# Optimization experiments

Hardware: AMD Instinct MI355X
Metric: run time of the kernel (lower is better)

The kernel has to match this reference:

```python
import jax, jax.numpy as jnp
import numpy as np

SR = 48000
TIME_LENGTH = 62400  # int(1.3 * 48000)
MAX_VOICES = 16


def _conv1d_same(x, k, b):
    # x: [B, L, Cin], k: [K, Cin, Cout] -> [B, L, Cout], keras Conv1D padding='same'
    y = jax.lax.conv_general_dilated(x, k, (1,), 'SAME', dimension_numbers=('NWC', 'WIO', 'NWC'))
    return y + b


def setup_inputs() -> dict:
    key = jax.random.key(0)
    ks = jax.random.split(key, 20)
    B, L, D, C = 16, 250, 128, 32
    V = MAX_VOICES
    din = D + C
    w = lambda k, s: jax.random.normal(k, s, jnp.float32) * 0.05
    inp = {}
    inp['base_signal'] = jax.random.normal(ks[0], (B, TIME_LENGTH), jnp.float32)
    inp['z'] = jax.random.normal(ks[1], (B, L, D), jnp.float32)
    inp['cond'] = jax.random.uniform(ks[2], (B, C), jnp.float32)
    inp['fundamental_freq'] = jax.random.uniform(ks[3], (B,), jnp.float32)
    # param_predictor: Dense(256)->Dense(128)->Dense(64)->Dense(4)
    inp['W1'] = w(ks[4], (din, 256)); inp['b1'] = jnp.zeros((256,), jnp.float32)
    inp['W2'] = w(ks[5], (256, 128)); inp['b2'] = jnp.zeros((128,), jnp.float32)
    inp['W3'] = w(ks[6], (128, 64));  inp['b3'] = jnp.zeros((64,), jnp.float32)
    inp['W4'] = w(ks[7], (64, 4));    inp['b4'] = jnp.zeros((4,), jnp.float32)
    # voice_gain_net: Conv1D(128,7)->Conv1D(64,5)->Conv1D(V,3), input channels = D + C
    inp['K1'] = w(ks[8], (7, din, 128)); inp['cb1'] = jnp.zeros((128,), jnp.float32)
    inp['K2'] = w(ks[9], (5, 128, 64));  inp['cb2'] = jnp.zeros((64,), jnp.float32)
    inp['K3'] = w(ks[10], (3, 64, V));   inp['cb3'] = jnp.zeros((V,), jnp.float32)
    return inp


def reference(base_signal, z, cond, fundamental_freq,
              W1, b1, W2, b2, W3, b3, W4, b4,
              K1, cb1, K2, cb2, K3, cb3):
    B, T = base_signal.shape
    L = z.shape[1]
    V = MAX_VOICES
    # ---- global param predictor ----
    z_global = jnp.mean(z, axis=1)
    x = jnp.concatenate([z_global, cond], axis=-1)
    h = jax.nn.relu(x @ W1 + b1)
    h = jax.nn.relu(h @ W2 + b2)
    h = jax.nn.relu(h @ W3 + b3)
    params = h @ W4 + b4  # [B,4]
    num_voices = 1.0 + 14.0 * jax.nn.sigmoid(params[:, 0:1])  # [B,1]
    detune_cents = params[:, 1:2] * 50.0                       # [B,1] (unused downstream, as in source)
    spread = jax.nn.sigmoid(params[:, 2:3])                    # [B,1]
    depth = jax.nn.sigmoid(params[:, 3:4]) * 0.5               # [B,1]
    # ---- per-voice gain envelopes at latent rate ----
    z_cond = jnp.concatenate([z, jnp.broadcast_to(cond[:, None, :], (B, L, cond.shape[-1]))], axis=-1)
    g = jax.nn.relu(_conv1d_same(z_cond, K1, cb1))
    g = jax.nn.relu(_conv1d_same(g, K2, cb2))
    g = _conv1d_same(g, K3, cb3)  # [B, L, V]
    # TF bilinear resize (half-pixel centers) L -> T along time axis
    scale = L / T
    src = jnp.clip((jnp.arange(T, dtype=jnp.float32) + 0.5) * scale - 0.5, 0.0, L - 1.0)
    i0 = jnp.floor(src).astype(jnp.int32)
    i1 = jnp.minimum(i0 + 1, L - 1)
    frac = (src - i0.astype(jnp.float32))[None, :, None]
    vg = g[:, i0, :] * (1.0 - frac) + g[:, i1, :] * frac
    voice_gains = jax.nn.softplus(vg)  # [B, T, V]
    # ---- 16-voice detune/roll/LFO-modulate/accumulate, vectorized over voices ----
    pos = (np.arange(V) - (V - 1) / 2.0) / V            # static [V]
    shifts = np.trunc(pos * 20.0).astype(np.int64)      # int() truncation as in source
    gidx = (np.arange(T)[None, :] - shifts[:, None]) % T  # static [V, T] gather for tf.roll
    shifted = base_signal[:, jnp.asarray(gidx)]         # [B, V, T]
    t = jnp.arange(T, dtype=jnp.float32) / SR
    lfo_freq = 3.0 + 0.3 * jnp.arange(V, dtype=jnp.float32)
    lfo = jnp.sin(2.0 * np.pi * lfo_freq[:, None] * t[None, :])  # [V, T]
    modulated = shifted * (1.0 + 0.2 * depth[:, 0][:, None, None] * lfo[None])  # [B, V, T]
    pan = 1.0 - jnp.abs(jnp.asarray(pos, dtype=jnp.float32))[None, :] * spread * 0.5  # [B, V]
    unison = jnp.einsum('bvt,btv,bv->bt', modulated, voice_gains, pan)  # [B, T]
    # ---- soft voice-count mask and normalization ----
    voice_mask = jax.nn.sigmoid((num_voices - jnp.arange(V, dtype=jnp.float32)[None, :]) * 2.0)  # [B, V]
    norm = jnp.sqrt(jnp.sum(voice_mask, axis=-1, keepdims=True) + 1e-6)  # [B, 1]
    gain_sum = jnp.einsum('btv,bv->bt', voice_gains, voice_mask)  # [B, T]
    return gain_sum / (norm + 1e-6) * unison
```

## Files before the change

### kernel.cpp

```cpp
#include <hip/hip_runtime.h>
#include <hip/hip_bf16.h>
#include <math.h>

#define L_LEN 250
#define D_DIM 128
#define C_DIM 32
#define DIN   160
#define NV    16
#define T_LEN 62400

__global__ __launch_bounds__(256) void zmean_kernel(const float* __restrict__ z,
                                                    float* __restrict__ zpart) {
    int b = blockIdx.x / 10, s = blockIdx.x % 10;
    int l0 = s * 25;
    int tid = threadIdx.x;
    int d4 = tid & 31, rg = tid >> 5;
    float4 acc = make_float4(0.f, 0.f, 0.f, 0.f);
    const float4* zp = (const float4*)(z + ((size_t)b * L_LEN + l0) * D_DIM) + d4;
    for (int r = rg; r < 25; r += 8) {
        float4 v = zp[(size_t)r * 32];
        acc.x += v.x; acc.y += v.y; acc.z += v.z; acc.w += v.w;
    }
    __shared__ float4 sm[8][32];
    sm[rg][d4] = acc;
    __syncthreads();
    if (rg == 0) {
        #pragma unroll
        for (int g = 1; g < 8; ++g) {
            float4 v = sm[g][d4];
            acc.x += v.x; acc.y += v.y; acc.z += v.z; acc.w += v.w;
        }
        ((float4*)(zpart + ((size_t)b * 10 + s) * 128))[d4] = acc;
    }
}

__global__ __launch_bounds__(256) void conv1_mlp_kernel(
        const float* __restrict__ z, const float* __restrict__ cond,
        const float* __restrict__ K1, float* __restrict__ parts1,
        const float* __restrict__ zpart,
        const float* __restrict__ W1, const float* __restrict__ b1,
        const float* __restrict__ W2, const float* __restrict__ b2,
        const float* __restrict__ W3, const float* __restrict__ b3,
        const float* __restrict__ W4, const float* __restrict__ b4,
        float* __restrict__ P) {
    int tid = threadIdx.x;
    if (blockIdx.x >= 1024) {
        int b = blockIdx.x - 1024;
        __shared__ float xb[DIN];
        __shared__ float h1[256];
        __shared__ float h2[128];
        __shared__ float h3[64];
        __shared__ float pr[4];
        if (tid < 128) {
            float s = 0.f;
            const float* zp = zpart + (size_t)b * 10 * 128 + tid;
            #pragma unroll
            for (int q = 0; q < 10; ++q) s += zp[q * 128];
            xb[tid] = s * (1.0f / (float)L_LEN);
        } else if (tid < DIN) {
            xb[tid] = cond[b * C_DIM + (tid - 128)];
        }
        __syncthreads();
        {
            float a0 = b1[tid], a1 = 0.f;
            #pragma unroll 8
            for (int i = 0; i < DIN; i += 2) {
                a0 = fmaf(xb[i],     W1[i * 256 + tid],       a0);
                a1 = fmaf(xb[i + 1], W1[(i + 1) * 256 + tid], a1);
            }
            h1[tid] = fmaxf(a0 + a1, 0.f);
        }
        __syncthreads();
        if (tid < 128) {
            float a0 = b2[tid], a1 = 0.f;
            #pragma unroll 8
            for (int i = 0; i < 256; i += 2) {
                a0 = fmaf(h1[i],     W2[i * 128 + tid],       a0);
                a1 = fmaf(h1[i + 1], W2[(i + 1) * 128 + tid], a1);
            }
            h2[tid] = fmaxf(a0 + a1, 0.f);
        }
        __syncthreads();
        if (tid < 64) {
            float a0 = b3[tid], a1 = 0.f;
            #pragma unroll 8
            for (int i = 0; i < 128; i += 2) {
                a0 = fmaf(h2[i],     W3[i * 64 + tid],       a0);
                a1 = fmaf(h2[i + 1], W3[(i + 1) * 64 + tid], a1);
            }
            h3[tid] = fmaxf(a0 + a1, 0.f);
        }
        __syncthreads();
        if (tid < 4) {
            float acc = b4[tid];
            #pragma unroll 8
            for (int i = 0; i < 64; ++i) acc = fmaf(h3[i], W4[i * 4 + tid], acc);
            pr[tid] = acc;
        }
        __syncthreads();
        if (tid == 0) {
            float num_voices = 1.0f + 14.0f / (1.0f + __expf(-pr[0]));
            float spread     = 1.0f / (1.0f + __expf(-pr[2]));
            float depth      = 0.5f / (1.0f + __expf(-pr[3]));
            float* Pb = P + b * 40;
            float msum = 0.f;
            for (int v = 0; v < NV; ++v) {
                float m = 1.0f / (1.0f + __expf(-(num_voices - (float)v) * 2.0f));
                msum += m;
                Pb[2 + v] = m;
                float pos = ((float)v - 7.5f) * (1.0f / 16.0f);
                Pb[2 + NV + v] = 1.0f - fabsf(pos) * spread * 0.5f;
            }
            float norm = sqrtf(msum + 1e-6f);
            Pb[0] = depth;
            Pb[1] = 1.0f / (norm + 1e-6f);
        }
        return;
    }
    int blk = blockIdx.x;
    int s  = blk >> 8;
    int b  = (blk >> 4) & 15;
    int lt = blk & 15;
    int l0 = lt * 16;
    __shared__ float smc[40][28];
    for (int idx = tid; idx < 22 * 40; idx += 256) {
        int pl = idx / 40;
        int il = idx - pl * 40;
        int p  = l0 - 3 + pl;
        int gi = s * 40 + il;
        float v = 0.f;
        if (p >= 0 && p < L_LEN)
            v = (gi < D_DIM) ? z[((size_t)b * L_LEN + p) * D_DIM + gi]
                             : cond[b * C_DIM + (gi - D_DIM)];
        smc[il][pl] = v;
    }
    __syncthreads();
    int oc = tid & 127;
    int lb = (tid >> 7) * 8;
    float acc[8];
    #pragma unroll
    for (int j = 0; j < 8; ++j) acc[j] = 0.f;
    const float* kbase = K1 + (size_t)(s * 40) * 128 + oc;
    for (int il = 0; il < 40; ++il) {
        float zr[16];
        *(float4*)&zr[0]  = *(const float4*)&smc[il][lb];
        *(float4*)&zr[4]  = *(const float4*)&smc[il][lb + 4];
        *(float4*)&zr[8]  = *(const float4*)&smc[il][lb + 8];
        *(float4*)&zr[12] = *(const float4*)&smc[il][lb + 12];
        const float* kp = kbase + (size_t)il * 128;
        #pragma unroll
        for (int tap = 0; tap < 7; ++tap) {
            float k = kp[(size_t)tap * DIN * 128];
            #pragma unroll
            for (int j = 0; j < 8; ++j) acc[j] = fmaf(zr[tap + j], k, acc[j]);
        }
    }
    float* po = parts1 + (size_t)s * (16 * L_LEN * 128) + ((size_t)b * L_LEN) * 128 + oc;
    #pragma unroll
    for (int j = 0; j < 8; ++j) {
        int l = l0 + lb + j;
        if (l < L_LEN) po[(size_t)l * 128] = acc[j];
    }
}

__global__ __launch_bounds__(256) void conv2_split_kernel(
        const float* __restrict__ parts1, const float* __restrict__ cb1,
        const float* __restrict__ K2, float* __restrict__ parts2) {
    int blk = blockIdx.x;
    int h  = blk >> 8;
    int b  = (blk >> 4) & 15;
    int lt = blk & 15;
    int l0 = lt * 16;
    int tid = threadIdx.x;
    const int PSTR = 16 * L_LEN * 128;
    __shared__ float sm[64][28];
    for (int idx = tid; idx < 20 * 64; idx += 256) {
        int pl = idx >> 6;
        int il = idx & 63;
        int p  = l0 - 2 + pl;
        int gi = h * 64 + il;
        float v = 0.f;
        if (p >= 0 && p < L_LEN) {
            size_t o = ((size_t)b * L_LEN + p) * 128 + gi;
            v = cb1[gi] + parts1[o] + parts1[o + PSTR] + parts1[o + 2 * PSTR] + parts1[o + 3 * PSTR];
            v = fmaxf(v, 0.f);
        }
        sm[il][pl] = v;
    }
    __syncthreads();
    int oc = tid & 63;
    int lb = (tid >> 6) * 4;
    float acc[4];
    #pragma unroll
    for (int j = 0; j < 4; ++j) acc[j] = 0.f;
    const float* kbase = K2 + (size_t)(h * 64) * 64 + oc;
    for (int il = 0; il < 64; ++il) {
        float zr[8];
        *(float4*)&zr[0] = *(const float4*)&sm[il][lb];
        *(float4*)&zr[4] = *(const float4*)&sm[il][lb + 4];
        const float* kp = kbase + (size_t)il * 64;
        #pragma unroll
        for (int tap = 0; tap < 5; ++tap) {
            float k = kp[(size_t)tap * 128 * 64];
            #pragma unroll
            for (int j = 0; j < 4; ++j) acc[j] = fmaf(zr[tap + j], k, acc[j]);
        }
    }
    float* po = parts2 + (size_t)h * (16 * L_LEN * 64) + ((size_t)b * L_LEN) * 64 + oc;
    #pragma unroll
    for (int j = 0; j < 4; ++j) {
        int l = l0 + lb + j;
        if (l < L_LEN) po[(size_t)l * 64] = acc[j];
    }
}

__global__ __launch_bounds__(256) void conv3_kernel(
        const float* __restrict__ parts2, const float* __restrict__ cb2,
        const float* __restrict__ K3, const float* __restrict__ cb3,
        float* __restrict__ g3) {
    int b  = blockIdx.x >> 4;
    int lt = blockIdx.x & 15;
    int l0 = lt * 16;
    int tid = threadIdx.x;
    const int PSTR2 = 16 * L_LEN * 64;
    __shared__ float sm2[18][68];
    __shared__ float k3t[16][196];
    for (int idx = tid; idx < 3 * 64 * 16; idx += 256) {
        int v  = idx & 15;
        int ti = idx >> 4;
        k3t[v][ti] = K3[ti * 16 + v];
    }
    for (int idx = tid; idx < 18 * 64; idx += 256) {
        int pl = idx >> 6;
        int i  = idx & 63;
        int p  = l0 - 1 + pl;
        float v = 0.f;
        if (p >= 0 && p < L_LEN) {
            size_t o = ((size_t)b * L_LEN + p) * 64 + i;
            v = fmaxf(cb2[i] + parts2[o] + parts2[o + PSTR2], 0.f);
        }
        sm2[pl][i] = v;
    }
    __syncthreads();
    int v  = tid & 15;
    int lq = tid >> 4;
    int l  = l0 + lq;
    float acc = cb3[v];
    #pragma unroll
    for (int tap = 0; tap < 3; ++tap) {
        #pragma unroll
        for (int i4 = 0; i4 < 16; ++i4) {
            float4 g = *(const float4*)&sm2[lq + tap][i4 * 4];
            float4 k = *(const float4*)&k3t[v][tap * 64 + i4 * 4];
            acc = fmaf(g.x, k.x, acc);
            acc = fmaf(g.y, k.y, acc);
            acc = fmaf(g.z, k.z, acc);
            acc = fmaf(g.w, k.w, acc);
        }
    }
    if (l < L_LEN) g3[((size_t)b * L_LEN + l) * NV + v] = acc;
}

__global__ __launch_bounds__(256) void main_kernel(
        const float* __restrict__ base, const float* __restrict__ g3,
        const float* __restrict__ P, float* __restrict__ out) {
    const int CB = (T_LEN + 255) / 256;
    int b = blockIdx.x / CB;
    int c = blockIdx.x % CB;
    int t = c * 256 + threadIdx.x;
    __shared__ float Pb[34];
    if (threadIdx.x < 34) Pb[threadIdx.x] = P[b * 40 + threadIdx.x];
    __syncthreads();
    if (t >= T_LEN) return;
    float depth = Pb[0];
    float coef  = Pb[1];
    const float scale = 250.0f / 62400.0f;
    float src = ((float)t + 0.5f) * scale - 0.5f;
    src = fminf(fmaxf(src, 0.0f), 249.0f);
    float fi0 = floorf(src);
    int i0 = (int)fi0;
    int i1 = min(i0 + 1, L_LEN - 1);
    float frac = src - fi0;
    const float4* r0 = (const float4*)(g3 + ((size_t)b * L_LEN + i0) * NV);
    const float4* r1 = (const float4*)(g3 + ((size_t)b * L_LEN + i1) * NV);
    float vg[16];
    #pragma unroll
    for (int q = 0; q < 4; ++q) {
        float4 a = r0[q];
        float4 d = r1[q];
        vg[q * 4 + 0] = fmaf(d.x - a.x, frac, a.x);
        vg[q * 4 + 1] = fmaf(d.y - a.y, frac, a.y);
        vg[q * 4 + 2] = fmaf(d.z - a.z, frac, a.z);
        vg[q * 4 + 3] = fmaf(d.w - a.w, frac, a.w);
    }
    float tsec = (float)t * (1.0f / 48000.0f);
    const float* bs = base + (size_t)b * T_LEN;
    const int shifts[NV] = {-9,-8,-6,-5,-4,-3,-1,0,0,1,3,4,5,6,8,9};
    float gain_sum = 0.f, uni = 0.f;
    #pragma unroll
    for (int v = 0; v < NV; ++v) {
        float x = vg[v];
        float sp = fmaxf(x, 0.f) + __logf(1.0f + __expf(-fabsf(x)));
        float fv = 3.0f + 0.3f * (float)v;
        float ph = fv * tsec;
        ph -= floorf(ph);
        float lfo = __sinf(6.283185307179586f * ph);
        int tb = t - shifts[v];
        if (tb < 0) tb += T_LEN; else if (tb >= T_LEN) tb -= T_LEN;
        float mod = bs[tb] * fmaf(0.2f * depth, lfo, 1.0f);
        gain_sum = fmaf(sp, Pb[2 + v], gain_sum);
        uni      = fmaf(mod * sp, Pb[2 + NV + v], uni);
    }
    out[(size_t)b * T_LEN + t] = gain_sum * coef * uni;
}

__global__ void params_kernel(const float* __restrict__ z, const float* __restrict__ cond,
                              const float* __restrict__ W1, const float* __restrict__ b1,
                              const float* __restrict__ W2, const float* __restrict__ b2,
                              const float* __restrict__ W3, const float* __restrict__ b3,
                              const float* __restrict__ W4, const float* __restrict__ b4,
                              float* __restrict__ P) {
    int b = blockIdx.x;
    int tid = threadIdx.x;
    __shared__ float xb[DIN];
    __shared__ float zp2[128];
    __shared__ float h1[256];
    __shared__ float h2[128];
    __shared__ float h3[64];
    __shared__ float pr[4];
    {
        int i = tid & 127, half = tid >> 7;
        const float* zp = z + (size_t)b * L_LEN * D_DIM + i;
        float s = 0.f;
        for (int l = half; l < L_LEN; l += 2) s += zp[(size_t)l * D_DIM];
        if (half) zp2[i] = s;
        __syncthreads();
        if (!half) xb[i] = (s + zp2[i]) * (1.0f / (float)L_LEN);
        if (tid >= 128 && tid < DIN) xb[tid] = cond[b * C_DIM + (tid - 128)];
    }
    __syncthreads();
    {
        float acc = b1[tid];
        for (int i = 0; i < DIN; ++i) acc = fmaf(xb[i], W1[i * 256 + tid], acc);
        h1[tid] = fmaxf(acc, 0.f);
    }
    __syncthreads();
    if (tid < 128) {
        float acc = b2[tid];
        for (int i = 0; i < 256; ++i) acc = fmaf(h1[i], W2[i * 128 + tid], acc);
        h2[tid] = fmaxf(acc, 0.f);
    }
    __syncthreads();
    if (tid < 64) {
        float acc = b3[tid];
        for (int i = 0; i < 128; ++i) acc = fmaf(h2[i], W3[i * 64 + tid], acc);
        h3[tid] = fmaxf(acc, 0.f);
    }
    __syncthreads();
    if (tid < 4) {
        float acc = b4[tid];
        for (int i = 0; i < 64; ++i) acc = fmaf(h3[i], W4[i * 4 + tid], acc);
        pr[tid] = acc;
    }
    __syncthreads();
    if (tid == 0) {
        float num_voices = 1.0f + 14.0f / (1.0f + __expf(-pr[0]));
        float spread     = 1.0f / (1.0f + __expf(-pr[2]));
        float depth      = 0.5f / (1.0f + __expf(-pr[3]));
        float* Pb = P + b * 40;
        float msum = 0.f;
        for (int v = 0; v < NV; ++v) {
            float m = 1.0f / (1.0f + __expf(-(num_voices - (float)v) * 2.0f));
            msum += m;
            Pb[2 + v] = m;
            float pos = ((float)v - 7.5f) * (1.0f / 16.0f);
            Pb[2 + NV + v] = 1.0f - fabsf(pos) * spread * 0.5f;
        }
        float norm = sqrtf(msum + 1e-6f);
        Pb[0] = depth;
        Pb[1] = 1.0f / (norm + 1e-6f);
    }
}

__global__ void conv1_mono_kernel(const float* __restrict__ z, const float* __restrict__ cond,
                                  const float* __restrict__ K1, const float* __restrict__ cb1,
                                  float* __restrict__ g1) {
    int b  = blockIdx.x >> 4;
    int lt = blockIdx.x & 15;
    int l0 = lt * 16;
    int tid = threadIdx.x;
    __shared__ float sm[DIN][22];
    for (int idx = tid; idx < 22 * DIN; idx += 256) {
        int pl = idx / DIN;
        int i  = idx - pl * DIN;
        int p  = l0 - 3 + pl;
        float v = 0.f;
        if (p >= 0 && p < L_LEN)
            v = (i < D_DIM) ? z[((size_t)b * L_LEN + p) * D_DIM + i]
                            : cond[b * C_DIM + (i - D_DIM)];
        sm[i][pl] = v;
    }
    __syncthreads();
    int oc = tid & 127;
    int lb = (tid >> 7) * 8;
    float bias = cb1[oc];
    float acc[8];
    #pragma unroll
    for (int j = 0; j < 8; ++j) acc[j] = bias;
    for (int i = 0; i < DIN; ++i) {
        float zr[14];
        #pragma unroll
        for (int q = 0; q < 14; ++q) zr[q] = sm[i][lb + q];
        #pragma unroll
        for (int tap = 0; tap < 7; ++tap) {
            float k = K1[(size_t)(tap * DIN + i) * 128 + oc];
            #pragma unroll
            for (int j = 0; j < 8; ++j) acc[j] = fmaf(zr[tap + j], k, acc[j]);
        }
    }
    #pragma unroll
    for (int j = 0; j < 8; ++j) {
        int l = l0 + lb + j;
        if (l < L_LEN) g1[((size_t)b * L_LEN + l) * 128 + oc] = fmaxf(acc[j], 0.f);
    }
}

__global__ void conv2_mono_kernel(const float* __restrict__ g1,
                                  const float* __restrict__ K2, const float* __restrict__ cb2,
                                  float* __restrict__ g2) {
    int b  = blockIdx.x >> 4;
    int lt = blockIdx.x & 15;
    int l0 = lt * 16;
    int tid = threadIdx.x;
    __shared__ float sm[128][20];
    for (int idx = tid; idx < 20 * 128; idx += 256) {
        int pl = idx >> 7;
        int i  = idx & 127;
        int p  = l0 - 2 + pl;
        float v = (p >= 0 && p < L_LEN) ? g1[((size_t)b * L_LEN + p) * 128 + i] : 0.f;
        sm[i][pl] = v;
    }
    __syncthreads();
    int oc = tid & 63;
    int lb = (tid >> 6) * 4;
    float bias = cb2[oc];
    float acc[4];
    #pragma unroll
    for (int j = 0; j < 4; ++j) acc[j] = bias;
    for (int i = 0; i < 128; ++i) {
        float zr[8];
        #pragma unroll
        for (int q = 0; q < 8; ++q) zr[q] = sm[i][lb + q];
        #pragma unroll
        for (int tap = 0; tap < 5; ++tap) {
            float k = K2[(size_t)(tap * 128 + i) * 64 + oc];
            #pragma unroll
            for (int j = 0; j < 4; ++j) acc[j] = fmaf(zr[tap + j], k, acc[j]);
        }
    }
    #pragma unroll
    for (int j = 0; j < 4; ++j) {
        int l = l0 + lb + j;
        if (l < L_LEN) g2[((size_t)b * L_LEN + l) * 64 + oc] = fmaxf(acc[j], 0.f);
    }
}

__global__ void conv3_mono_kernel(const float* __restrict__ g2,
                                  const float* __restrict__ K3, const float* __restrict__ cb3,
                                  float* __restrict__ g3) {
    int b  = blockIdx.x >> 4;
    int lt = blockIdx.x & 15;
    int l0 = lt * 16;
    int tid = threadIdx.x;
    int v  = tid & 15;
    int ll = tid >> 4;
    int l  = l0 + ll;
    if (l >= L_LEN) return;
    float acc = cb3[v];
    #pragma unroll
    for (int tap = 0; tap < 3; ++tap) {
        int p = l + tap - 1;
        if (p < 0 || p >= L_LEN) continue;
        const float* gp = g2 + ((size_t)b * L_LEN + p) * 64;
        #pragma unroll
        for (int i = 0; i < 64; ++i) acc = fmaf(gp[i], K3[(size_t)(tap * 64 + i) * 16 + v], acc);
    }
    g3[((size_t)b * L_LEN + l) * 16 + v] = acc;
}

extern "C" void kernel_launch(void* const* d_in, const int* in_sizes, int n_in,
                              void* d_out, int out_size, void* d_ws, size_t ws_size,
                              hipStream_t stream) {
    const float* base = (const float*)d_in[0];
    const float* z    = (const float*)d_in[1];
    const float* cond = (const float*)d_in[2];
    const float* W1 = (const float*)d_in[4];  const float* b1 = (const float*)d_in[5];
    const float* W2 = (const float*)d_in[6];  const float* b2 = (const float*)d_in[7];
    const float* W3 = (const float*)d_in[8];  const float* b3 = (const float*)d_in[9];
    const float* W4 = (const float*)d_in[10]; const float* b4 = (const float*)d_in[11];
    const float* K1 = (const float*)d_in[12]; const float* cb1 = (const float*)d_in[13];
    const float* K2 = (const float*)d_in[14]; const float* cb2 = (const float*)d_in[15];
    const float* K3 = (const float*)d_in[16]; const float* cb3 = (const float*)d_in[17];
    float* out = (float*)d_out;

    int B = in_sizes[0] / T_LEN;
    const int CB = (T_LEN + 255) / 256;

    float* ws = (float*)d_ws;
    const size_t P1 = (size_t)16 * L_LEN * 128;
    const size_t P2 = (size_t)16 * L_LEN * 64;
    const size_t ZP = (size_t)16 * 10 * 128;
    size_t need = (1024 + ZP + 4 * P1 + 2 * P2 + (size_t)16 * L_LEN * NV) * sizeof(float);

    float* P = ws;
    if (ws_size >= need) {
        float* zpart  = ws + 1024;
        float* parts1 = zpart + ZP;
        float* parts2 = parts1 + 4 * P1;
        float* g3     = parts2 + 2 * P2;
        zmean_kernel<<<B * 10, 256, 0, stream>>>(z, zpart);
        conv1_mlp_kernel<<<4 * B * 16 + B, 256, 0, stream>>>(
            z, cond, K1, parts1, zpart, W1, b1, W2, b2, W3, b3, W4, b4, P);
        conv2_split_kernel<<<2 * B * 16, 256, 0, stream>>>(parts1, cb1, K2, parts2);
        conv3_kernel<<<B * 16, 256, 0, stream>>>(parts2, cb2, K3, cb3, g3);
        main_kernel<<<B * CB, 256, 0, stream>>>(base, g3, P, out);
    } else {
        float* g1 = ws + 1024;
        float* g2 = g1 + (size_t)B * L_LEN * 128;
        float* g3 = g2 + (size_t)B * L_LEN * 64;
        params_kernel<<<B, 256, 0, stream>>>(z, cond, W1, b1, W2, b2, W3, b3, W4, b4, P);
        conv1_mono_kernel<<<B * 16, 256, 0, stream>>>(z, cond, K1, cb1, g1);
        conv2_mono_kernel<<<B * 16, 256, 0, stream>>>(g1, K2, cb2, g2);
        conv3_mono_kernel<<<B * 16, 256, 0, stream>>>(g2, K3, cb3, g3);
        main_kernel<<<B * CB, 256, 0, stream>>>(base, g3, P, out);
    }
}
```

Measured before the change: 67.51 us.

## Fuse conv3 into main kernel and fold z-mean into MLP blocks

Drops the separate z-mean kernel: the MLP blocks, now the first 16 blocks of the conv1 grid, compute the mean over L themselves. Fuses the conv3 stage into the main synthesis kernel. Each block recomputes the few g3 rows its time segment needs from parts2 into shared memory, so the g3 buffer round trip and a launch disappear. The LFO now uses the hardware sin intrinsic, which takes a phase in revolutions and skips the 2π multiply. In exchange, every block reloads and transposes K3 and redundantly computes conv3 rows, and the serial MLP blocks each do the full 250-row z reduction.

Measured after the change: 65.28 us. -3.3%, faster.

```diff
diff --git a/kernel.cpp b/kernel.cpp
--- a/kernel.cpp
+++ b/kernel.cpp
@@ -8,56 +8,47 @@
 #define DIN   160
 #define NV    16
 #define T_LEN 62400
-
-__global__ __launch_bounds__(256) void zmean_kernel(const float* __restrict__ z,
-                                                    float* __restrict__ zpart) {
-    int b = blockIdx.x / 10, s = blockIdx.x % 10;
-    int l0 = s * 25;
-    int tid = threadIdx.x;
-    int d4 = tid & 31, rg = tid >> 5;
-    float4 acc = make_float4(0.f, 0.f, 0.f, 0.f);
-    const float4* zp = (const float4*)(z + ((size_t)b * L_LEN + l0) * D_DIM) + d4;
-    for (int r = rg; r < 25; r += 8) {
-        float4 v = zp[(size_t)r * 32];
-        acc.x += v.x; acc.y += v.y; acc.z += v.z; acc.w += v.w;
-    }
-    __shared__ float4 sm[8][32];
-    sm[rg][d4] = acc;
-    __syncthreads();
-    if (rg == 0) {
-        #pragma unroll
-        for (int g = 1; g < 8; ++g) {
-            float4 v = sm[g][d4];
-            acc.x += v.x; acc.y += v.y; acc.z += v.z; acc.w += v.w;
-        }
-        ((float4*)(zpart + ((size_t)b * 10 + s) * 128))[d4] = acc;
-    }
-}
+#define CB    244
 
 __global__ __launch_bounds__(256) void conv1_mlp_kernel(
         const float* __restrict__ z, const float* __restrict__ cond,
         const float* __restrict__ K1, float* __restrict__ parts1,
-        const float* __restrict__ zpart,
         const float* __restrict__ W1, const float* __restrict__ b1,
         const float* __restrict__ W2, const float* __restrict__ b2,
         const float* __restrict__ W3, const float* __restrict__ b3,
         const float* __restrict__ W4, const float* __restrict__ b4,
         float* __restrict__ P) {
     int tid = threadIdx.x;
-    if (blockIdx.x >= 1024) {
-        int b = blockIdx.x - 1024;
+    if (blockIdx.x < 16) {
+        int b = blockIdx.x;
         __shared__ float xb[DIN];
+        __shared__ float4 sm4[8][32];
         __shared__ float h1[256];
         __shared__ float h2[128];
         __shared__ float h3[64];
         __shared__ float pr[4];
-        if (tid < 128) {
-            float s = 0.f;
-            const float* zp = zpart + (size_t)b * 10 * 128 + tid;
+        {
+            int c4 = tid & 31, rg = tid >> 5;
+            const float4* zp = (const float4*)(z + (size_t)b * L_LEN * D_DIM) + c4;
+            float4 acc = make_float4(0.f, 0.f, 0.f, 0.f);
+            for (int r = rg; r < L_LEN; r += 8) {
+                float4 v = zp[(size_t)r * 32];
+                acc.x += v.x; acc.y += v.y; acc.z += v.z; acc.w += v.w;
+            }
+            sm4[rg][c4] = acc;
+        }
+        __syncthreads();
+        if (tid < 32) {
+            float4 acc = sm4[0][tid];
             #pragma unroll
-            for (int q = 0; q < 10; ++q) s += zp[q * 128];
-            xb[tid] = s * (1.0f / (float)L_LEN);
-        } else if (tid < DIN) {
+            for (int g = 1; g < 8; ++g) {
+                float4 v = sm4[g][tid];
+                acc.x += v.x; acc.y += v.y; acc.z += v.z; acc.w += v.w;
+            }
+            const float inv = 1.0f / (float)L_LEN;
+            acc.x *= inv; acc.y *= inv; acc.z *= inv; acc.w *= inv;
+            ((float4*)xb)[tid] = acc;
+        } else if (tid >= 128 && tid < DIN) {
             xb[tid] = cond[b * C_DIM + (tid - 128)];
         }
         __syncthreads();
@@ -117,7 +108,7 @@
         }
         return;
     }
-    int blk = blockIdx.x;
+    int blk = blockIdx.x - 16;
     int s  = blk >> 8;
     int b  = (blk >> 4) & 15;
     int lt = blk & 15;
@@ -214,57 +205,288 @@
     }
 }
 
-__global__ __launch_bounds__(256) void conv3_kernel(
-        const float* __restrict__ parts2, const float* __restrict__ cb2,
+__global__ __launch_bounds__(256) void conv3_main_kernel(
+        const float* __restrict__ base, const float* __restrict__ parts2,
+        const float* __restrict__ cb2,
         const float* __restrict__ K3, const float* __restrict__ cb3,
-        float* __restrict__ g3) {
-    int b  = blockIdx.x >> 4;
-    int lt = blockIdx.x & 15;
-    int l0 = lt * 16;
+        const float* __restrict__ P, float* __restrict__ out) {
+    int b = blockIdx.x / CB;
+    int c = blockIdx.x % CB;
+    int t0 = c * 256;
     int tid = threadIdx.x;
     const int PSTR2 = 16 * L_LEN * 64;
-    __shared__ float sm2[18][68];
+    const float scale = 250.0f / 62400.0f;
+
     __shared__ float k3t[16][196];
+    __shared__ float sA[6][68];
+    __shared__ float g3loc[4][17];
+    __shared__ float Pb[34];
+
+    float src0 = ((float)t0 + 0.5f) * scale - 0.5f;
+    src0 = fminf(fmaxf(src0, 0.0f), 249.0f);
+    int L0 = (int)floorf(src0);
+
+    if (tid < 34) Pb[tid] = P[b * 40 + tid];
     for (int idx = tid; idx < 3 * 64 * 16; idx += 256) {
         int v  = idx & 15;
         int ti = idx >> 4;
         k3t[v][ti] = K3[ti * 16 + v];
     }
-    for (int idx = tid; idx < 18 * 64; idx += 256) {
+    for (int idx = tid; idx < 6 * 64; idx += 256) {
         int pl = idx >> 6;
         int i  = idx & 63;
-        int p  = l0 - 1 + pl;
+        int p  = L0 - 1 + pl;
         float v = 0.f;
         if (p >= 0 && p < L_LEN) {
             size_t o = ((size_t)b * L_LEN + p) * 64 + i;
             v = fmaxf(cb2[i] + parts2[o] + parts2[o + PSTR2], 0.f);
         }
-        sm2[pl][i] = v;
-    }
-    __syncthreads();
+        sA[pl][i] = v;
+    }
+    __syncthreads();
+
+    {
+        int seg = tid & 3;
+        int v   = (tid >> 2) & 15;
+        int r   = tid >> 6;
+        float acc = 0.f;
+        #pragma unroll
+        for (int tap = 0; tap < 3; ++tap) {
+            const float* gr = &sA[r + tap][seg * 16];
+            const float* kr = &k3t[v][tap * 64 + seg * 16];
+            #pragma unroll
+            for (int j = 0; j < 4; ++j) {
+                float4 g = *(const float4*)&gr[j * 4];
+                float4 k = *(const float4*)&kr[j * 4];
+                acc = fmaf(g.x, k.x, acc);
+                acc = fmaf(g.y, k.y, acc);
+                acc = fmaf(g.z, k.z, acc);
+                acc = fmaf(g.w, k.w, acc);
+            }
+        }
+        acc += __shfl_xor(acc, 1);
+        acc += __shfl_xor(acc, 2);
+        if (seg == 0) g3loc[r][v] = acc + cb3[v];
+    }
+    __syncthreads();
+
+    int t = t0 + tid;
+    if (t >= T_LEN) return;
+    float depth = Pb[0];
+    float coef  = Pb[1];
+    float src = ((float)t + 0.5f) * scale - 0.5f;
+    src = fminf(fmaxf(src, 0.0f), 249.0f);
+    float fi0 = floorf(src);
+    int i0 = (int)fi0;
+    int i1 = min(i0 + 1, L_LEN - 1);
+    float frac = src - fi0;
+    int r0 = i0 - L0;
+    int r1 = i1 - L0;
+    float vg[16];
+    #pragma unroll
+    for (int v = 0; v < NV; ++v) {
+        float a = g3loc[r0][v];
+        float d = g3loc[r1][v];
+        vg[v] = fmaf(d - a, frac, a);
+    }
+    float tsec = (float)t * (1.0f / 48000.0f);
+    const float* bs = base + (size_t)b * T_LEN;
+    const int shifts[NV] = {-9,-8,-6,-5,-4,-3,-1,0,0,1,3,4,5,6,8,9};
+    float gain_sum = 0.f, uni = 0.f;
+    #pragma unroll
+    for (int v = 0; v < NV; ++v) {
+        float x = vg[v];
+        float sp = fmaxf(x, 0.f) + __logf(1.0f + __expf(-fabsf(x)));
+        float fv = 3.0f + 0.3f * (float)v;
+        float ph = fv * tsec;
+        ph -= floorf(ph);
+        float lfo = __builtin_amdgcn_sinf(ph);
+        int tb = t - shifts[v];
+        if (tb < 0) tb += T_LEN; else if (tb >= T_LEN) tb -= T_LEN;
+        float mod = bs[tb] * fmaf(0.2f * depth, lfo, 1.0f);
+        gain_sum = fmaf(sp, Pb[2 + v], gain_sum);
+        uni      = fmaf(mod * sp, Pb[2 + NV + v], uni);
+    }
+    out[(size_t)b * T_LEN + t] = gain_sum * coef * uni;
+}
+
+__global__ void params_kernel(const float* __restrict__ z, const float* __restrict__ cond,
+                              const float* __restrict__ W1, const float* __restrict__ b1,
+                              const float* __restrict__ W2, const float* __restrict__ b2,
+                              const float* __restrict__ W3, const float* __restrict__ b3,
+                              const float* __restrict__ W4, const float* __restrict__ b4,
+                              float* __restrict__ P) {
+    int b = blockIdx.x;
+    int tid = threadIdx.x;
+    __shared__ float xb[DIN];
+    __shared__ float zp2[128];
+    __shared__ float h1[256];
+    __shared__ float h2[128];
+    __shared__ float h3[64];
+    __shared__ float pr[4];
+    {
+        int i = tid & 127, half = tid >> 7;
+        const float* zp = z + (size_t)b * L_LEN * D_DIM + i;
+        float s = 0.f;
+        for (int l = half; l < L_LEN; l += 2) s += zp[(size_t)l * D_DIM];
+        if (half) zp2[i] = s;
+        __syncthreads();
+        if (!half) xb[i] = (s + zp2[i]) * (1.0f / (float)L_LEN);
+        if (tid >= 128 && tid < DIN) xb[tid] = cond[b * C_DIM + (tid - 128)];
+    }
+    __syncthreads();
+    {
+        float acc = b1[tid];
+        for (int i = 0; i < DIN; ++i) acc = fmaf(xb[i], W1[i * 256 + tid], acc);
+        h1[tid] = fmaxf(acc, 0.f);
+    }
+    __syncthreads();
+    if (tid < 128) {
+        float acc = b2[tid];
+        for (int i = 0; i < 256; ++i) acc = fmaf(h1[i], W2[i * 128 + tid], acc);
+        h2[tid] = fmaxf(acc, 0.f);
+    }
+    __syncthreads();
+    if (tid < 64) {
+        float acc = b3[tid];
+        for (int i = 0; i < 128; ++i) acc = fmaf(h2[i], W3[i * 64 + tid], acc);
+        h3[tid] = fmaxf(acc, 0.f);
+    }
+    __syncthreads();
+    if (tid < 4) {
+        float acc = b4[tid];
+        for (int i = 0; i < 64; ++i) acc = fmaf(h3[i], W4[i * 4 + tid], acc);
+        pr[tid] = acc;
+    }
+    __syncthreads();
+    if (tid == 0) {
+        float num_voices = 1.0f + 14.0f / (1.0f + __expf(-pr[0]));
+        float spread     = 1.0f / (1.0f + __expf(-pr[2]));
+        float depth      = 0.5f / (1.0f + __expf(-pr[3]));
+        float* Pb = P + b * 40;
+        float msum = 0.f;
+        for (int v = 0; v < NV; ++v) {
+            float m = 1.0f / (1.0f + __expf(-(num_voices - (float)v) * 2.0f));
+            msum += m;
+            Pb[2 + v] = m;
+            float pos = ((float)v - 7.5f) * (1.0f / 16.0f);
+            Pb[2 + NV + v] = 1.0f - fabsf(pos) * spread * 0.5f;
+        }
+        float norm = sqrtf(msum + 1e-6f);
+        Pb[0] = depth;
+        Pb[1] = 1.0f / (norm + 1e-6f);
+    }
+}
+
+__global__ void conv1_mono_kernel(const float* __restrict__ z, const float* __restrict__ cond,
+                                  const float* __restrict__ K1, const float* __restrict__ cb1,
+                                  float* __restrict__ g1) {
+    int b  = blockIdx.x >> 4;
+    int lt = blockIdx.x & 15;
+    int l0 = lt * 16;
+    int tid = threadIdx.x;
+    __shared__ float sm[DIN][22];
+    for (int idx = tid; idx < 22 * DIN; idx += 256) {
+        int pl = idx / DIN;
+        int i  = idx - pl * DIN;
+        int p  = l0 - 3 + pl;
+        float v = 0.f;
+        if (p >= 0 && p < L_LEN)
+            v = (i < D_DIM) ? z[((size_t)b * L_LEN + p) * D_DIM + i]
+                            : cond[b * C_DIM + (i - D_DIM)];
+        sm[i][pl] = v;
+    }
+    __syncthreads();
+    int oc = tid & 127;
+    int lb = (tid >> 7) * 8;
+    float bias = cb1[oc];
+    float acc[8];
+    #pragma unroll
+    for (int j = 0; j < 8; ++j) acc[j] = bias;
+    for (int i = 0; i < DIN; ++i) {
+        float zr[14];
+        #pragma unroll
+        for (int q = 0; q < 14; ++q) zr[q] = sm[i][lb + q];
+        #pragma unroll
+        for (int tap = 0; tap < 7; ++tap) {
+            float k = K1[(size_t)(tap * DIN + i) * 128 + oc];
+            #pragma unroll
+            for (int j = 0; j < 8; ++j) acc[j] = fmaf(zr[tap + j], k, acc[j]);
+        }
+    }
+    #pragma unroll
+    for (int j = 0; j < 8; ++j) {
+        int l = l0 + lb + j;
+        if (l < L_LEN) g1[((size_t)b * L_LEN + l) * 128 + oc] = fmaxf(acc[j], 0.f);
+    }
+}
+
+__global__ void conv2_mono_kernel(const float* __restrict__ g1,
+                                  const float* __restrict__ K2, const float* __restrict__ cb2,
+                                  float* __restrict__ g2) {
+    int b  = blockIdx.x >> 4;
+    int lt = blockIdx.x & 15;
+    int l0 = lt * 16;
+    int tid = threadIdx.x;
+    __shared__ float sm[128][20];
+    for (int idx = tid; idx < 20 * 128; idx += 256) {
+        int pl = idx >> 7;
+        int i  = idx & 127;
+        int p  = l0 - 2 + pl;
+        float v = (p >= 0 && p < L_LEN) ? g1[((size_t)b * L_LEN + p) * 128 + i] : 0.f;
+        sm[i][pl] = v;
+    }
+    __syncthreads();
+    int oc = tid & 63;
+    int lb = (tid >> 6) * 4;
+    float bias = cb2[oc];
+    float acc[4];
+    #pragma unroll
+    for (int j = 0; j < 4; ++j) acc[j] = bias;
+    for (int i = 0; i < 128; ++i) {
+        float zr[8];
+        #pragma unroll
+        for (int q = 0; q < 8; ++q) zr[q] = sm[i][lb + q];
+        #pragma unroll
+        for (int tap = 0; tap < 5; ++tap) {
+            float k = K2[(size_t)(tap * 128 + i) * 64 + oc];
+            #pragma unroll
+            for (int j = 0; j < 4; ++j) acc[j] = fmaf(zr[tap + j], k, acc[j]);
+        }
+    }
+    #pragma unroll
+    for (int j = 0; j < 4; ++j) {
+        int l = l0 + lb + j;
+        if (l < L_LEN) g2[((size_t)b * L_LEN + l) * 64 + oc] = fmaxf(acc[j], 0.f);
+    }
+}
+
+__global__ void conv3_mono_kernel(const float* __restrict__ g2,
+                                  const float* __restrict__ K3, const float* __restrict__ cb3,
+                                  float* __restrict__ g3) {
+    int b  = blockIdx.x >> 4;
+    int lt = blockIdx.x & 15;
+    int l0 = lt * 16;
+    int tid = threadIdx.x;
     int v  = tid & 15;
-    int lq = tid >> 4;
-    int l  = l0 + lq;
+    int ll = tid >> 4;
+    int l  = l0 + ll;
+    if (l >= L_LEN) return;
     float acc = cb3[v];
     #pragma unroll
     for (int tap = 0; tap < 3; ++tap) {
-        #pragma unroll
-        for (int i4 = 0; i4 < 16; ++i4) {
-            float4 g = *(const float4*)&sm2[lq + tap][i4 * 4];
-            float4 k = *(const float4*)&k3t[v][tap * 64 + i4 * 4];
-            acc = fmaf(g.x, k.x, acc);
-            acc = fmaf(g.y, k.y, acc);
-            acc = fmaf(g.z, k.z, acc);
-            acc = fmaf(g.w, k.w, acc);
-        }
-    }
-    if (l < L_LEN) g3[((size_t)b * L_LEN + l) * NV + v] = acc;
-}
-
-__global__ __launch_bounds__(256) void main_kernel(
+        int p = l + tap - 1;
+        if (p < 0 || p >= L_LEN) continue;
+        const float* gp = g2 + ((size_t)b * L_LEN + p) * 64;
+        #pragma unroll
+        for (int i = 0; i < 64; ++i) acc = fmaf(gp[i], K3[(size_t)(tap * 64 + i) * 16 + v], acc);
+    }
+    g3[((size_t)b * L_LEN + l) * 16 + v] = acc;
+}
+
+__global__ __launch_bounds__(256) void main_mono_kernel(
         const float* __restrict__ base, const float* __restrict__ g3,
         const float* __restrict__ P, float* __restrict__ out) {
-    const int CB = (T_LEN + 255) / 256;
     int b = blockIdx.x / CB;
     int c = blockIdx.x % CB;
     int t = c * 256 + threadIdx.x;
@@ -304,7 +526,7 @@
         float fv = 3.0f + 0.3f * (float)v;
         float ph = fv * tsec;
         ph -= floorf(ph);
-        float lfo = __sinf(6.283185307179586f * ph);
+        float lfo = __builtin_amdgcn_sinf(ph);
         int tb = t - shifts[v];
         if (tb < 0) tb += T_LEN; else if (tb >= T_LEN) tb -= T_LEN;
         float mod = bs[tb] * fmaf(0.2f * depth, lfo, 1.0f);
@@ -312,180 +534,6 @@
         uni      = fmaf(mod * sp, Pb[2 + NV + v], uni);
     }
     out[(size_t)b * T_LEN + t] = gain_sum * coef * uni;
-}
-
-__global__ void params_kernel(const float* __restrict__ z, const float* __restrict__ cond,
-                              const float* __restrict__ W1, const float* __restrict__ b1,
-                              const float* __restrict__ W2, const float* __restrict__ b2,
-                              const float* __restrict__ W3, const float* __restrict__ b3,
-                              const float* __restrict__ W4, const float* __restrict__ b4,
-                              float* __restrict__ P) {
-    int b = blockIdx.x;
-    int tid = threadIdx.x;
-    __shared__ float xb[DIN];
-    __shared__ float zp2[128];
-    __shared__ float h1[256];
-    __shared__ float h2[128];
-    __shared__ float h3[64];
-    __shared__ float pr[4];
-    {
-        int i = tid & 127, half = tid >> 7;
-        const float* zp = z + (size_t)b * L_LEN * D_DIM + i;
-        float s = 0.f;
-        for (int l = half; l < L_LEN; l += 2) s += zp[(size_t)l * D_DIM];
-        if (half) zp2[i] = s;
-        __syncthreads();
-        if (!half) xb[i] = (s + zp2[i]) * (1.0f / (float)L_LEN);
-        if (tid >= 128 && tid < DIN) xb[tid] = cond[b * C_DIM + (tid - 128)];
-    }
-    __syncthreads();
-    {
-        float acc = b1[tid];
-        for (int i = 0; i < DIN; ++i) acc = fmaf(xb[i], W1[i * 256 + tid], acc);
-        h1[tid] = fmaxf(acc, 0.f);
-    }
-    __syncthreads();
-    if (tid < 128) {
-        float acc = b2[tid];
-        for (int i = 0; i < 256; ++i) acc = fmaf(h1[i], W2[i * 128 + tid], acc);
-        h2[tid] = fmaxf(acc, 0.f);
-    }
-    __syncthreads();
-    if (tid < 64) {
-        float acc = b3[tid];
-        for (int i = 0; i < 128; ++i) acc = fmaf(h2[i], W3[i * 64 + tid], acc);
-        h3[tid] = fmaxf(acc, 0.f);
-    }
-    __syncthreads();
-    if (tid < 4) {
-        float acc = b4[tid];
-        for (int i = 0; i < 64; ++i) acc = fmaf(h3[i], W4[i * 4 + tid], acc);
-        pr[tid] = acc;
-    }
-    __syncthreads();
-    if (tid == 0) {
-        float num_voices = 1.0f + 14.0f / (1.0f + __expf(-pr[0]));
-        float spread     = 1.0f / (1.0f + __expf(-pr[2]));
-        float depth      = 0.5f / (1.0f + __expf(-pr[3]));
-        float* Pb = P + b * 40;
-        float msum = 0.f;
-        for (int v = 0; v < NV; ++v) {
-            float m = 1.0f / (1.0f + __expf(-(num_voices - (float)v) * 2.0f));
-            msum += m;
-            Pb[2 + v] = m;
-            float pos = ((float)v - 7.5f) * (1.0f / 16.0f);
-            Pb[2 + NV + v] = 1.0f - fabsf(pos) * spread * 0.5f;
-        }
-        float norm = sqrtf(msum + 1e-6f);
-        Pb[0] = depth;
-        Pb[1] = 1.0f / (norm + 1e-6f);
-    }
-}
-
-__global__ void conv1_mono_kernel(const float* __restrict__ z, const float* __restrict__ cond,
-                                  const float* __restrict__ K1, const float* __restrict__ cb1,
-                                  float* __restrict__ g1) {
-    int b  = blockIdx.x >> 4;
-    int lt = blockIdx.x & 15;
-    int l0 = lt * 16;
-    int tid = threadIdx.x;
-    __shared__ float sm[DIN][22];
-    for (int idx = tid; idx < 22 * DIN; idx += 256) {
-        int pl = idx / DIN;
-        int i  = idx - pl * DIN;
-        int p  = l0 - 3 + pl;
-        float v = 0.f;
-        if (p >= 0 && p < L_LEN)
-            v = (i < D_DIM) ? z[((size_t)b * L_LEN + p) * D_DIM + i]
-                            : cond[b * C_DIM + (i - D_DIM)];
-        sm[i][pl] = v;
-    }
-    __syncthreads();
-    int oc = tid & 127;
-    int lb = (tid >> 7) * 8;
-    float bias = cb1[oc];
-    float acc[8];
-    #pragma unroll
-    for (int j = 0; j < 8; ++j) acc[j] = bias;
-    for (int i = 0; i < DIN; ++i) {
-        float zr[14];
-        #pragma unroll
-        for (int q = 0; q < 14; ++q) zr[q] = sm[i][lb + q];
-        #pragma unroll
-        for (int tap = 0; tap < 7; ++tap) {
-            float k = K1[(size_t)(tap * DIN + i) * 128 + oc];
-            #pragma unroll
-            for (int j = 0; j < 8; ++j) acc[j] = fmaf(zr[tap + j], k, acc[j]);
-        }
-    }
-    #pragma unroll
-    for (int j = 0; j < 8; ++j) {
-        int l = l0 + lb + j;
-        if (l < L_LEN) g1[((size_t)b * L_LEN + l) * 128 + oc] = fmaxf(acc[j], 0.f);
-    }
-}
-
-__global__ void conv2_mono_kernel(const float* __restrict__ g1,
-                                  const float* __restrict__ K2, const float* __restrict__ cb2,
-                                  float* __restrict__ g2) {
-    int b  = blockIdx.x >> 4;
-    int lt = blockIdx.x & 15;
-    int l0 = lt * 16;
-    int tid = threadIdx.x;
-    __shared__ float sm[128][20];
-    for (int idx = tid; idx < 20 * 128; idx += 256) {
-        int pl = idx >> 7;
-        int i  = idx & 127;
-        int p  = l0 - 2 + pl;
-        float v = (p >= 0 && p < L_LEN) ? g1[((size_t)b * L_LEN + p) * 128 + i] : 0.f;
-        sm[i][pl] = v;
-    }
-    __syncthreads();
-    int oc = tid & 63;
-    int lb = (tid >> 6) * 4;
-    float bias = cb2[oc];
-    float acc[4];
-    #pragma unroll
-    for (int j = 0; j < 4; ++j) acc[j] = bias;
-    for (int i = 0; i < 128; ++i) {
-        float zr[8];
-        #pragma unroll
-        for (int q = 0; q < 8; ++q) zr[q] = sm[i][lb + q];
-        #pragma unroll
-        for (int tap = 0; tap < 5; ++tap) {
-            float k = K2[(size_t)(tap * 128 + i) * 64 + oc];
-            #pragma unroll
-            for (int j = 0; j < 4; ++j) acc[j] = fmaf(zr[tap + j], k, acc[j]);
-        }
-    }
-    #pragma unroll
-    for (int j = 0; j < 4; ++j) {
-        int l = l0 + lb + j;
-        if (l < L_LEN) g2[((size_t)b * L_LEN + l) * 64 + oc] = fmaxf(acc[j], 0.f);
-    }
-}
-
-__global__ void conv3_mono_kernel(const float* __restrict__ g2,
-                                  const float* __restrict__ K3, const float* __restrict__ cb3,
-                                  float* __restrict__ g3) {
-    int b  = blockIdx.x >> 4;
-    int lt = blockIdx.x & 15;
-    int l0 = lt * 16;
-    int tid = threadIdx.x;
-    int v  = tid & 15;
-    int ll = tid >> 4;
-    int l  = l0 + ll;
-    if (l >= L_LEN) return;
-    float acc = cb3[v];
-    #pragma unroll
-    for (int tap = 0; tap < 3; ++tap) {
-        int p = l + tap - 1;
-        if (p < 0 || p >= L_LEN) continue;
-        const float* gp = g2 + ((size_t)b * L_LEN + p) * 64;
-        #pragma unroll
-        for (int i = 0; i < 64; ++i) acc = fmaf(gp[i], K3[(size_t)(tap * 64 + i) * 16 + v], acc);
-    }
-    g3[((size_t)b * L_LEN + l) * 16 + v] = acc;
 }
 
 extern "C" void kernel_launch(void* const* d_in, const int* in_sizes, int n_in,
@@ -504,26 +552,20 @@
     float* out = (float*)d_out;
 
     int B = in_sizes[0] / T_LEN;
-    const int CB = (T_LEN + 255) / 256;
 
     float* ws = (float*)d_ws;
     const size_t P1 = (size_t)16 * L_LEN * 128;
     const size_t P2 = (size_t)16 * L_LEN * 64;
-    const size_t ZP = (size_t)16 * 10 * 128;
-    size_t need = (1024 + ZP + 4 * P1 + 2 * P2 + (size_t)16 * L_LEN * NV) * sizeof(float);
+    size_t need = (1024 + 4 * P1 + 2 * P2) * sizeof(float);
 
     float* P = ws;
     if (ws_size >= need) {
-        float* zpart  = ws + 1024;
-        float* parts1 = zpart + ZP;
+        float* parts1 = ws + 1024;
         float* parts2 = parts1 + 4 * P1;
-        float* g3     = parts2 + 2 * P2;
-        zmean_kernel<<<B * 10, 256, 0, stream>>>(z, zpart);
-        conv1_mlp_kernel<<<4 * B * 16 + B, 256, 0, stream>>>(
-            z, cond, K1, parts1, zpart, W1, b1, W2, b2, W3, b3, W4, b4, P);
+        conv1_mlp_kernel<<<16 + 4 * B * 16, 256, 0, stream>>>(
+            z, cond, K1, parts1, W1, b1, W2, b2, W3, b3, W4, b4, P);
         conv2_split_kernel<<<2 * B * 16, 256, 0, stream>>>(parts1, cb1, K2, parts2);
-        conv3_kernel<<<B * 16, 256, 0, stream>>>(parts2, cb2, K3, cb3, g3);
-        main_kernel<<<B * CB, 256, 0, stream>>>(base, g3, P, out);
+        conv3_main_kernel<<<B * CB, 256, 0, stream>>>(base, parts2, cb2, K3, cb3, P, out);
     } else {
         float* g1 = ws + 1024;
         float* g2 = g1 + (size_t)B * L_LEN * 128;
@@ -532,6 +574,6 @@
         conv1_mono_kernel<<<B * 16, 256, 0, stream>>>(z, cond, K1, cb1, g1);
         conv2_mono_kernel<<<B * 16, 256, 0, stream>>>(g1, K2, cb2, g2);
         conv3_mono_kernel<<<B * 16, 256, 0, stream>>>(g2, K3, cb3, g3);
-        main_kernel<<<B * CB, 256, 0, stream>>>(base, g3, P, out);
-    }
-}
+        main_mono_kernel<<<B * CB, 256, 0, stream>>>(base, g3, P, out);
+    }
+}
```
